# Optimization experiments

Measured on AMD Instinct MI355X. Metric: run time of the kernel, lower is better.

Reference implementation:

```python
import jax, jax.numpy as jnp
import numpy as np

K, N = 4096, 4096
GROUP_SIZE = 64
N_GROUPS = N // GROUP_SIZE
B, S = 4, 2048
NBITS = 4


def setup_inputs() -> dict:
    key = jax.random.key(0)
    ks = jax.random.split(key, 7)
    x = jax.random.normal(ks[0], (B, S, N), dtype=jnp.float32)
    # per-group scales/zeros broadcast over the group_size axis
    scales = jax.random.uniform(ks[1], (K, N_GROUPS, 1), dtype=jnp.float32, minval=0.001, maxval=0.05)
    zeros = jax.random.uniform(ks[2], (K, N_GROUPS, 1), dtype=jnp.float32, minval=0.0, maxval=2.0 ** NBITS - 1)
    mu1 = jax.random.uniform(ks[3], (N,), dtype=jnp.float32, minval=0.5, maxval=1.5)
    mu2 = jax.random.uniform(ks[4], (K,), dtype=jnp.float32, minval=0.5, maxval=1.5)
    bias = jax.random.normal(ks[5], (K,), dtype=jnp.float32)
    W_q = jax.random.randint(ks[6], (K, N), 0, 2 ** NBITS, dtype=jnp.int32)
    return {"x": x, "scales": scales, "zeros": zeros, "mu1": mu1, "mu2": mu2, "bias": bias, "W_q": W_q}


def reference(x, scales, zeros, mu1, mu2, bias, W_q):
    # dequantize: per-group (Q - zero) * scale, then Sinkhorn rescale mu2 (rows) * mu1 (cols)
    k, n = W_q.shape
    n_groups = scales.shape[1]
    Qg = W_q.astype(jnp.float32).reshape(k, n_groups, -1)  # [K, G, gs]
    W_deq = ((Qg - zeros) * scales).reshape(k, n) * mu2[:, None] * mu1[None, :]
    W_deq = W_deq.astype(x.dtype)
    # nn.functional.linear: x @ W^T + b
    return jnp.einsum('bsn,kn->bsk', x, W_deq) + bias
```

## Files before the change

### kernel.cpp

```cpp
#include <hip/hip_runtime.h>
#include <hip/hip_bf16.h>
#include <stdint.h>
#include <type_traits>

typedef unsigned short u16;
typedef __bf16 bf16x8 __attribute__((ext_vector_type(8)));
typedef float f32x4 __attribute__((ext_vector_type(4)));

#define M_TOT 8192
#define N_TOT 4096
#define K_TOT 4096
#define BM 256
#define BN 256
#define BK 64
#define NT 64

#define HALF_EL 8192
#define B_OFF   16384
#define SLOT_EL 32768

template <int V> using ic = std::integral_constant<int, V>;
template <bool V> using bc = std::integral_constant<bool, V>;

__device__ __forceinline__ u16 f2bf(float f) {
    union { float f; uint32_t u; } v; v.f = f;
    uint32_t u = v.u;
    return (u16)((u + 0x7fffu + ((u >> 16) & 1u)) >> 16);
}

__global__ __launch_bounds__(256) void cvt_x_kernel(const float* __restrict__ x,
                                                    u16* __restrict__ xb) {
    const int i = blockIdx.x * blockDim.x + threadIdx.x;
    const float4* p = (const float4*)x + (size_t)i * 2;
    float4 v0 = p[0], v1 = p[1];
    uint4 o;
    o.x = (uint32_t)f2bf(v0.x) | ((uint32_t)f2bf(v0.y) << 16);
    o.y = (uint32_t)f2bf(v0.z) | ((uint32_t)f2bf(v0.w) << 16);
    o.z = (uint32_t)f2bf(v1.x) | ((uint32_t)f2bf(v1.y) << 16);
    o.w = (uint32_t)f2bf(v1.z) | ((uint32_t)f2bf(v1.w) << 16);
    *((uint4*)(xb + (size_t)i * 8)) = o;
}

__global__ __launch_bounds__(256) void deq_w_kernel(const int* __restrict__ wq,
                                                    const float* __restrict__ scales,
                                                    const float* __restrict__ zeros,
                                                    const float* __restrict__ mu1,
                                                    const float* __restrict__ mu2,
                                                    u16* __restrict__ wb) {
    const int i = blockIdx.x * blockDim.x + threadIdx.x;
    const int k  = i >> 9;
    const int n0 = (i & 511) << 3;
    const int g  = n0 >> 6;
    const float z  = zeros[k * 64 + g];
    const float sm = scales[k * 64 + g] * mu2[k];
    const int4* qp = (const int4*)(wq + (size_t)k * N_TOT + n0);
    int4 q0 = qp[0], q1 = qp[1];
    const float4* mp = (const float4*)(mu1 + n0);
    float4 u0 = mp[0], u1 = mp[1];
    uint4 o;
    o.x = (uint32_t)f2bf(((float)q0.x - z) * sm * u0.x) |
          ((uint32_t)f2bf(((float)q0.y - z) * sm * u0.y) << 16);
    o.y = (uint32_t)f2bf(((float)q0.z - z) * sm * u0.z) |
          ((uint32_t)f2bf(((float)q0.w - z) * sm * u0.w) << 16);
    o.z = (uint32_t)f2bf(((float)q1.x - z) * sm * u1.x) |
          ((uint32_t)f2bf(((float)q1.y - z) * sm * u1.y) << 16);
    o.w = (uint32_t)f2bf(((float)q1.z - z) * sm * u1.z) |
          ((uint32_t)f2bf(((float)q1.w - z) * sm * u1.w) << 16);
    *((uint4*)(wb + (size_t)k * N_TOT + n0)) = o;
}

__global__ __launch_bounds__(512, 2) void gemm_kernel(const u16* __restrict__ Xb,
                                                      const u16* __restrict__ Wb,
                                                      const float* __restrict__ bias,
                                                      float* __restrict__ out) {
    __shared__ __align__(16) u16 lds[2 * SLOT_EL];

    const int bid = blockIdx.x;
    const int cpx = gridDim.x >> 3;
    const int swz = (bid & 7) * cpx + (bid >> 3);
    const int bm = swz >> 4;
    const int bn = swz & 15;

    const int tid  = threadIdx.x;
    const int w    = tid >> 6;
    const int lane = tid & 63;
    const int wm = w >> 2, wn = w & 3;

    const int scol = (((lane & 7) ^ (lane >> 3)) << 3);
    const u16* aT = Xb + (size_t)(bm * BM + w * 16 + (lane >> 3)) * N_TOT + scol;
    const u16* bT = Wb + (size_t)(bn * BN + w * 16 + (lane >> 3)) * N_TOT + scol;

    u16* const sdA = &lds[w * 1024];
    u16* const sdB = &lds[B_OFF + w * 1024];

    auto gload = [](const u16* s, u16* d) {
        __builtin_amdgcn_global_load_lds(
            (const __attribute__((address_space(1))) uint32_t*)s,
            (__attribute__((address_space(3))) uint32_t*)d, 16, 0, 0);
    };
    auto stA = [&](auto SlC, auto Hc, auto Dc) {
        const u16* s = aT + (size_t)(Hc.value * 128) * N_TOT + Dc.value;
        u16* d = sdA + SlC.value * SLOT_EL + Hc.value * HALF_EL;
        gload(s, d); gload(s + (size_t)8 * N_TOT, d + 512);
    };
    auto stB = [&](auto SlC, auto Hc, auto Dc) {
        const u16* s = bT + (size_t)(Hc.value * 128) * N_TOT + Dc.value;
        u16* d = sdB + SlC.value * SLOT_EL + Hc.value * HALF_EL;
        gload(s, d); gload(s + (size_t)8 * N_TOT, d + 512);
    };

    const int cc0 = (((lane >> 4) << 3)) ^ ((lane & 7) << 3);
    const int rA  = ((wm << 4) + (lane & 15)) << 6;
    const int rB  = ((wn << 4) + (lane & 15)) << 6;
    const u16* pAk[2][2];
    const u16* pBk[2][2];
    pAk[0][0] = &lds[rA + cc0];
    pAk[0][1] = &lds[rA + (cc0 ^ 32)];
    pAk[1][0] = pAk[0][0] + SLOT_EL;
    pAk[1][1] = pAk[0][1] + SLOT_EL;
    pBk[0][0] = &lds[B_OFF + rB + cc0];
    pBk[0][1] = &lds[B_OFF + rB + (cc0 ^ 32)];
    pBk[1][0] = pBk[0][0] + SLOT_EL;
    pBk[1][1] = pBk[0][1] + SLOT_EL;

    f32x4 acc[2][2][4][2] = {};
    bf16x8 afLo[4][2], afHi[4][2];
    bf16x8 bf0[2][2], bf1[2][2];

    auto rd_afLo = [&](auto SlC) {
        constexpr int SL = SlC.value;
        #pragma unroll
        for (int j = 0; j < 4; ++j) {
            afLo[j][0] = *(const bf16x8*)(pAk[SL][0] + j * 2048);
            afLo[j][1] = *(const bf16x8*)(pAk[SL][1] + j * 2048);
        }
    };
    auto rd_afHi = [&](auto SlC) {
        constexpr int SL = SlC.value;
        #pragma unroll
        for (int j = 0; j < 4; ++j) {
            afHi[j][0] = *(const bf16x8*)(pAk[SL][0] + HALF_EL + j * 2048);
            afHi[j][1] = *(const bf16x8*)(pAk[SL][1] + HALF_EL + j * 2048);
        }
    };
    auto rd_bf0 = [&](auto SlC) {
        constexpr int SL = SlC.value;
        #pragma unroll
        for (int j2 = 0; j2 < 2; ++j2) {
            bf0[j2][0] = *(const bf16x8*)(pBk[SL][0] + j2 * 4096);
            bf0[j2][1] = *(const bf16x8*)(pBk[SL][1] + j2 * 4096);
        }
    };
    auto rd_bf1 = [&](auto SlC) {
        constexpr int SL = SlC.value;
        #pragma unroll
        for (int j2 = 0; j2 < 2; ++j2) {
            bf1[j2][0] = *(const bf16x8*)(pBk[SL][0] + HALF_EL + j2 * 4096);
            bf1[j2][1] = *(const bf16x8*)(pBk[SL][1] + HALF_EL + j2 * 4096);
        }
    };

    auto vmw = [](auto Vc) {
        constexpr int V = Vc.value;
        if constexpr (V == 8)      asm volatile("s_waitcnt vmcnt(8)" ::: "memory");
        else if constexpr (V == 4) asm volatile("s_waitcnt vmcnt(4)" ::: "memory");
        else if constexpr (V == 0) asm volatile("s_waitcnt vmcnt(0)" ::: "memory");
    };

    #define MFMA_CLUSTER(A, B, MH, NH)                                          \
        __builtin_amdgcn_s_setprio(1);                                          \
        _Pragma("unroll")                                                       \
        for (int ks = 0; ks < 2; ++ks)                                          \
            _Pragma("unroll")                                                   \
            for (int j = 0; j < 4; ++j)                                         \
                _Pragma("unroll")                                               \
                for (int j2 = 0; j2 < 2; ++j2)                                  \
                    acc[MH][NH][j][j2] = __builtin_amdgcn_mfma_f32_16x16x32_bf16(\
                        A[j][ks], B[j2][ks], acc[MH][NH][j][j2], 0, 0, 0);      \
        __builtin_amdgcn_s_setprio(0);

    auto ktile = [&](auto SlC, auto St0, auto St1, auto Rd23,
                     auto Vm1, auto Vm3, auto D0, auto D1) {
        constexpr int SL = SlC.value;
        rd_bf1(SlC);
        if constexpr (St0.value) { stA(ic<SL ^ 1>{}, ic<1>{}, D0);
                                   stB(ic<SL ^ 1>{}, ic<1>{}, D0); }
        __builtin_amdgcn_s_barrier();
        MFMA_CLUSTER(afLo, bf0, 0, 0)
        __builtin_amdgcn_s_barrier();
        rd_afHi(SlC);
        if constexpr (St1.value) { stA(SlC, ic<0>{}, D1);
                                   stB(SlC, ic<0>{}, D1); }
        __builtin_amdgcn_s_barrier();
        MFMA_CLUSTER(afLo, bf1, 0, 1)
        vmw(Vm1);
        __builtin_amdgcn_s_barrier();
        if constexpr (Rd23.value) rd_afLo(ic<SL ^ 1>{});
        __builtin_amdgcn_s_barrier();
        MFMA_CLUSTER(afHi, bf1, 1, 1)
        __builtin_amdgcn_s_barrier();
        MFMA_CLUSTER(afHi, bf0, 1, 0)
        if constexpr (Rd23.value) rd_bf0(ic<SL ^ 1>{});
        vmw(Vm3);
        __builtin_amdgcn_s_barrier();
    };

    stA(ic<0>{}, ic<0>{}, ic<0>{});  stB(ic<0>{}, ic<0>{}, ic<0>{});
    stA(ic<0>{}, ic<1>{}, ic<0>{});  stB(ic<0>{}, ic<1>{}, ic<0>{});
    stA(ic<1>{}, ic<0>{}, ic<BK>{}); stB(ic<1>{}, ic<0>{}, ic<BK>{});
    asm volatile("s_waitcnt vmcnt(4)" ::: "memory");
    __builtin_amdgcn_s_barrier();
    rd_afLo(ic<0>{});
    rd_bf0(ic<0>{});

    for (int it = 0; it < 31; ++it) {
        ktile(ic<0>{}, bc<true>{}, bc<true>{}, bc<true>{},
              ic<8>{}, ic<4>{}, ic<BK>{}, ic<2 * BK>{});
        ktile(ic<1>{}, bc<true>{}, bc<true>{}, bc<true>{},
              ic<8>{}, ic<4>{}, ic<2 * BK>{}, ic<3 * BK>{});
        aT += 2 * BK;
        bT += 2 * BK;
    }
    ktile(ic<0>{}, bc<true>{}, bc<false>{}, bc<true>{},
          ic<4>{}, ic<0>{}, ic<BK>{}, ic<0>{});
    ktile(ic<1>{}, bc<false>{}, bc<false>{}, bc<false>{},
          ic<-1>{}, ic<-1>{}, ic<0>{}, ic<0>{});

    #undef MFMA_CLUSTER

    #pragma unroll
    for (int mh_ = 0; mh_ < 2; ++mh_)
        #pragma unroll
        for (int j = 0; j < 4; ++j)
            #pragma unroll
            for (int rr = 0; rr < 4; ++rr) {
                const int row = bm * BM + mh_ * 128 + j * 32 + wm * 16 + ((lane >> 4) << 2) + rr;
                float* orow = out + (size_t)row * K_TOT;
                #pragma unroll
                for (int nh_ = 0; nh_ < 2; ++nh_)
                    #pragma unroll
                    for (int j2 = 0; j2 < 2; ++j2) {
                        const int col = bn * BN + nh_ * 128 + j2 * 64 + wn * 16 + (lane & 15);
                        orow[col] = acc[mh_][nh_][j][j2][rr] + bias[col];
                    }
            }
}

extern "C" void kernel_launch(void* const* d_in, const int* in_sizes, int n_in,
                              void* d_out, int out_size, void* d_ws, size_t ws_size,
                              hipStream_t stream) {
    const float* x      = (const float*)d_in[0];
    const float* scales = (const float*)d_in[1];
    const float* zeros  = (const float*)d_in[2];
    const float* mu1    = (const float*)d_in[3];
    const float* mu2    = (const float*)d_in[4];
    const float* bias   = (const float*)d_in[5];
    const int*   wq     = (const int*)d_in[6];
    float* out = (float*)d_out;

    u16* xb = (u16*)d_ws;
    u16* wb = (u16*)d_ws + (size_t)M_TOT * N_TOT;

    cvt_x_kernel<<<(M_TOT * N_TOT / 8) / 256, 256, 0, stream>>>(x, xb);
    deq_w_kernel<<<(K_TOT * N_TOT / 8) / 256, 256, 0, stream>>>(wq, scales, zeros, mu1, mu2, wb);
    gemm_kernel<<<(M_TOT / BM) * (K_TOT / BN), 512, 0, stream>>>(xb, wb, bias, out);
}
```

Measured before the change: 291.4 us.

## Cut per-ktile barriers from six to two and use XOR-toggled LDS offsets

Restructures the main K-loop schedule so each k-tile has two workgroup barriers instead of six. MFMA clusters now run back-to-back with the LDS fragment reads and the async global-to-LDS stores placed between them, fenced by sched_barrier. LDS slot addressing switches from a pointer table indexed by a constant slot to byte offsets flipped with XOR each tile. The vmcnt waits are moved and retuned to match. The risk is a race on the double-buffered LDS slots if the reduced barriers do not fully order the reads and the overwrites.

```diff
diff --git a/kernel.cpp b/kernel.cpp
--- a/kernel.cpp
+++ b/kernel.cpp
@@ -18,6 +18,7 @@
 #define HALF_EL 8192
 #define B_OFF   16384
 #define SLOT_EL 32768
+#define SLOT_BYTES 65536
 
 template <int V> using ic = std::integral_constant<int, V>;
 template <bool V> using bc = std::integral_constant<bool, V>;
@@ -112,59 +113,45 @@
     const int cc0 = (((lane >> 4) << 3)) ^ ((lane & 7) << 3);
     const int rA  = ((wm << 4) + (lane & 15)) << 6;
     const int rB  = ((wn << 4) + (lane & 15)) << 6;
-    const u16* pAk[2][2];
-    const u16* pBk[2][2];
-    pAk[0][0] = &lds[rA + cc0];
-    pAk[0][1] = &lds[rA + (cc0 ^ 32)];
-    pAk[1][0] = pAk[0][0] + SLOT_EL;
-    pAk[1][1] = pAk[0][1] + SLOT_EL;
-    pBk[0][0] = &lds[B_OFF + rB + cc0];
-    pBk[0][1] = &lds[B_OFF + rB + (cc0 ^ 32)];
-    pBk[1][0] = pBk[0][0] + SLOT_EL;
-    pBk[1][1] = pBk[0][1] + SLOT_EL;
+    int oAa = (rA + cc0) * 2;
+    int oAb = (rA + (cc0 ^ 32)) * 2;
+    int oBa = (B_OFF + rB + cc0) * 2;
+    int oBb = (B_OFF + rB + (cc0 ^ 32)) * 2;
+    const char* const ldsc = (const char*)lds;
 
     f32x4 acc[2][2][4][2] = {};
     bf16x8 afLo[4][2], afHi[4][2];
     bf16x8 bf0[2][2], bf1[2][2];
 
-    auto rd_afLo = [&](auto SlC) {
-        constexpr int SL = SlC.value;
+    auto rd_afLo_next = [&]() {
+        const int xa = oAa ^ SLOT_BYTES, xb2 = oAb ^ SLOT_BYTES;
         #pragma unroll
         for (int j = 0; j < 4; ++j) {
-            afLo[j][0] = *(const bf16x8*)(pAk[SL][0] + j * 2048);
-            afLo[j][1] = *(const bf16x8*)(pAk[SL][1] + j * 2048);
-        }
-    };
-    auto rd_afHi = [&](auto SlC) {
-        constexpr int SL = SlC.value;
+            afLo[j][0] = *(const bf16x8*)(ldsc + xa + j * 4096);
+            afLo[j][1] = *(const bf16x8*)(ldsc + xb2 + j * 4096);
+        }
+    };
+    auto rd_bf0_next = [&]() {
+        const int xa = oBa ^ SLOT_BYTES, xb2 = oBb ^ SLOT_BYTES;
+        #pragma unroll
+        for (int j2 = 0; j2 < 2; ++j2) {
+            bf0[j2][0] = *(const bf16x8*)(ldsc + xa + j2 * 8192);
+            bf0[j2][1] = *(const bf16x8*)(ldsc + xb2 + j2 * 8192);
+        }
+    };
+    auto rd_afHi_cur = [&]() {
         #pragma unroll
         for (int j = 0; j < 4; ++j) {
-            afHi[j][0] = *(const bf16x8*)(pAk[SL][0] + HALF_EL + j * 2048);
-            afHi[j][1] = *(const bf16x8*)(pAk[SL][1] + HALF_EL + j * 2048);
-        }
-    };
-    auto rd_bf0 = [&](auto SlC) {
-        constexpr int SL = SlC.value;
+            afHi[j][0] = *(const bf16x8*)(ldsc + oAa + 16384 + j * 4096);
+            afHi[j][1] = *(const bf16x8*)(ldsc + oAb + 16384 + j * 4096);
+        }
+    };
+    auto rd_bf1_cur = [&]() {
         #pragma unroll
         for (int j2 = 0; j2 < 2; ++j2) {
-            bf0[j2][0] = *(const bf16x8*)(pBk[SL][0] + j2 * 4096);
-            bf0[j2][1] = *(const bf16x8*)(pBk[SL][1] + j2 * 4096);
-        }
-    };
-    auto rd_bf1 = [&](auto SlC) {
-        constexpr int SL = SlC.value;
-        #pragma unroll
-        for (int j2 = 0; j2 < 2; ++j2) {
-            bf1[j2][0] = *(const bf16x8*)(pBk[SL][0] + HALF_EL + j2 * 4096);
-            bf1[j2][1] = *(const bf16x8*)(pBk[SL][1] + HALF_EL + j2 * 4096);
-        }
-    };
-
-    auto vmw = [](auto Vc) {
-        constexpr int V = Vc.value;
-        if constexpr (V == 8)      asm volatile("s_waitcnt vmcnt(8)" ::: "memory");
-        else if constexpr (V == 4) asm volatile("s_waitcnt vmcnt(4)" ::: "memory");
-        else if constexpr (V == 0) asm volatile("s_waitcnt vmcnt(0)" ::: "memory");
+            bf1[j2][0] = *(const bf16x8*)(ldsc + oBa + 16384 + j2 * 8192);
+            bf1[j2][1] = *(const bf16x8*)(ldsc + oBb + 16384 + j2 * 8192);
+        }
     };
 
     #define MFMA_CLUSTER(A, B, MH, NH)                                          \
@@ -179,30 +166,30 @@
                         A[j][ks], B[j2][ks], acc[MH][NH][j][j2], 0, 0, 0);      \
         __builtin_amdgcn_s_setprio(0);
 
-    auto ktile = [&](auto SlC, auto St0, auto St1, auto Rd23,
-                     auto Vm1, auto Vm3, auto D0, auto D1) {
+    auto ktile = [&](auto SlC, auto St0, auto St2, auto RdN,
+                     auto V1c, auto V3c, auto D0, auto D1) {
         constexpr int SL = SlC.value;
-        rd_bf1(SlC);
+        rd_bf1_cur();
         if constexpr (St0.value) { stA(ic<SL ^ 1>{}, ic<1>{}, D0);
                                    stB(ic<SL ^ 1>{}, ic<1>{}, D0); }
+        MFMA_CLUSTER(afLo, bf0, 0, 0)
+        rd_afHi_cur();
+        MFMA_CLUSTER(afLo, bf1, 0, 1)
+        if constexpr (V1c.value == 4) asm volatile("s_waitcnt vmcnt(4)" ::: "memory");
+        else if constexpr (V1c.value == 0) asm volatile("s_waitcnt vmcnt(0)" ::: "memory");
         __builtin_amdgcn_s_barrier();
-        MFMA_CLUSTER(afLo, bf0, 0, 0)
+        __builtin_amdgcn_sched_barrier(0);
+        if constexpr (RdN.value) rd_afLo_next();
+        if constexpr (St2.value) { stA(SlC, ic<0>{}, D1);
+                                   stB(SlC, ic<0>{}, D1); }
+        MFMA_CLUSTER(afHi, bf1, 1, 1)
+        MFMA_CLUSTER(afHi, bf0, 1, 0)
+        if constexpr (RdN.value) rd_bf0_next();
+        if constexpr (V3c.value == 4) asm volatile("s_waitcnt vmcnt(4)" ::: "memory");
+        else if constexpr (V3c.value == 0) asm volatile("s_waitcnt vmcnt(0)" ::: "memory");
         __builtin_amdgcn_s_barrier();
-        rd_afHi(SlC);
-        if constexpr (St1.value) { stA(SlC, ic<0>{}, D1);
-                                   stB(SlC, ic<0>{}, D1); }
-        __builtin_amdgcn_s_barrier();
-        MFMA_CLUSTER(afLo, bf1, 0, 1)
-        vmw(Vm1);
-        __builtin_amdgcn_s_barrier();
-        if constexpr (Rd23.value) rd_afLo(ic<SL ^ 1>{});
-        __builtin_amdgcn_s_barrier();
-        MFMA_CLUSTER(afHi, bf1, 1, 1)
-        __builtin_amdgcn_s_barrier();
-        MFMA_CLUSTER(afHi, bf0, 1, 0)
-        if constexpr (Rd23.value) rd_bf0(ic<SL ^ 1>{});
-        vmw(Vm3);
-        __builtin_amdgcn_s_barrier();
+        __builtin_amdgcn_sched_barrier(0);
+        oAa ^= SLOT_BYTES; oAb ^= SLOT_BYTES; oBa ^= SLOT_BYTES; oBb ^= SLOT_BYTES;
     };
 
     stA(ic<0>{}, ic<0>{}, ic<0>{});  stB(ic<0>{}, ic<0>{}, ic<0>{});
@@ -210,14 +197,25 @@
     stA(ic<1>{}, ic<0>{}, ic<BK>{}); stB(ic<1>{}, ic<0>{}, ic<BK>{});
     asm volatile("s_waitcnt vmcnt(4)" ::: "memory");
     __builtin_amdgcn_s_barrier();
-    rd_afLo(ic<0>{});
-    rd_bf0(ic<0>{});
+    __builtin_amdgcn_sched_barrier(0);
+    {
+        #pragma unroll
+        for (int j = 0; j < 4; ++j) {
+            afLo[j][0] = *(const bf16x8*)(ldsc + oAa + j * 4096);
+            afLo[j][1] = *(const bf16x8*)(ldsc + oAb + j * 4096);
+        }
+        #pragma unroll
+        for (int j2 = 0; j2 < 2; ++j2) {
+            bf0[j2][0] = *(const bf16x8*)(ldsc + oBa + j2 * 8192);
+            bf0[j2][1] = *(const bf16x8*)(ldsc + oBb + j2 * 8192);
+        }
+    }
 
     for (int it = 0; it < 31; ++it) {
         ktile(ic<0>{}, bc<true>{}, bc<true>{}, bc<true>{},
-              ic<8>{}, ic<4>{}, ic<BK>{}, ic<2 * BK>{});
+              ic<4>{}, ic<4>{}, ic<BK>{}, ic<2 * BK>{});
         ktile(ic<1>{}, bc<true>{}, bc<true>{}, bc<true>{},
-              ic<8>{}, ic<4>{}, ic<2 * BK>{}, ic<3 * BK>{});
+              ic<4>{}, ic<4>{}, ic<2 * BK>{}, ic<3 * BK>{});
         aT += 2 * BK;
         bT += 2 * BK;
     }
```

Result: faster. 265.5 us (-8.9%).
